# Performance work log

Hardware: AMD Instinct MI355X
Metric: run time of the kernel (lower is better)

## Reference

```python
import jax, jax.numpy as jnp
import numpy as np

TEMPERATURE = 0.5
SCALE_LOSS = 1.0 / 32.0
LAMBDA = 0.0039


def setup_inputs() -> dict:
    key = jax.random.key(0)
    z = jax.random.normal(key, (4096, 6, 256), dtype=jnp.float32)
    return {"z": z}


def reference(z):
    B, V = z.shape[0], z.shape[1]
    # [B, V, ...] -> [V, B, D], L2-normalize embeddings
    zv = z.reshape(B, V, -1).transpose(1, 0, 2)
    zn = zv / jnp.linalg.norm(zv, axis=-1, keepdims=True)

    # Positive error: per-sample cross-view similarity [B, V, V]
    sim_pos = jnp.einsum('vbd,wbd->bvw', zn, zn)
    pos = jnp.exp((1.0 - sim_pos) / TEMPERATURE).mean(axis=(1, 2))  # [B]

    # Negative error: per-view within-batch similarity [V, B, B]
    sim_neg = jnp.exp(jnp.einsum('vbd,vcd->vbc', zn, zn) / TEMPERATURE)
    offdiag_mask = ~jnp.eye(B, dtype=bool)  # [B, B]
    off_mean = jnp.where(offdiag_mask[None], sim_neg, 0.0).sum(-1) / (B - 1)  # [V, B]
    neg = off_mean.sum(0)  # [B], accumulated over views

    return jnp.sum(pos) * SCALE_LOSS + LAMBDA * jnp.sum(neg)
```

## Files before the change

### kernel.cpp

```cpp
#include <hip/hip_runtime.h>
#include <cstdint>
#include <cstddef>

#define B_N 4096
#define V_N 6
#define D_N 256
#define NTILE 528
#define NBLK (NTILE * V_N)

typedef int i32x4 __attribute__((ext_vector_type(4)));

#define QC 298.0f
#define INV_C2_X2 (2.0f / (QC * QC))

__device__ __forceinline__ void async_load16(void* lds, const void* gmem) {
  __builtin_amdgcn_global_load_lds(
      (const __attribute__((address_space(1))) unsigned int*)gmem,
      (__attribute__((address_space(3))) unsigned int*)lds,
      16, 0, 0);
}

__global__ __launch_bounds__(256) void norm_pos_kernel(
    const float* __restrict__ z, signed char* __restrict__ znb,
    float* __restrict__ pos_part) {
  const int lane = threadIdx.x & 63;
  const int w = threadIdx.x >> 6;
  const int b = blockIdx.x * 4 + w;

  const float4* zb4 = (const float4*)(z + (size_t)b * (V_N * D_N));
  float4 x[V_N];
#pragma unroll
  for (int v = 0; v < V_N; ++v) x[v] = zb4[v * 64 + lane];

  float s[21];
  {
    int p = 0;
#pragma unroll
    for (int v = 0; v < V_N; ++v)
#pragma unroll
      for (int u = v; u < V_N; ++u) {
        s[p] = x[v].x * x[u].x + x[v].y * x[u].y +
               x[v].z * x[u].z + x[v].w * x[u].w;
        ++p;
      }
  }
#pragma unroll
  for (int off = 1; off < 64; off <<= 1)
#pragma unroll
    for (int q = 0; q < 21; ++q)
      s[q] += __shfl_xor(s[q], off);

  const int selfidx[V_N] = {0, 6, 11, 15, 18, 20};
  float inv[V_N];
#pragma unroll
  for (int v = 0; v < V_N; ++v) inv[v] = rsqrtf(s[selfidx[v]]);

#pragma unroll
  for (int v = 0; v < V_N; ++v) {
    const float sc = inv[v] * QC;
    int q0 = (int)rintf(fminf(127.0f, fmaxf(-127.0f, x[v].x * sc)));
    int q1 = (int)rintf(fminf(127.0f, fmaxf(-127.0f, x[v].y * sc)));
    int q2 = (int)rintf(fminf(127.0f, fmaxf(-127.0f, x[v].z * sc)));
    int q3 = (int)rintf(fminf(127.0f, fmaxf(-127.0f, x[v].w * sc)));
    int packed = (q0 & 255) | ((q1 & 255) << 8) | ((q2 & 255) << 16)
               | ((q3 & 255) << 24);
    ((int*)(znb + ((size_t)v * B_N + b) * D_N))[lane] = packed;
  }

  float psum = 0.0f;
  {
    int p = 0;
#pragma unroll
    for (int v = 0; v < V_N; ++v)
#pragma unroll
      for (int u = v; u < V_N; ++u) {
        if (u > v) psum += __expf(2.0f * (1.0f - s[p] * inv[v] * inv[u]));
        ++p;
      }
  }
  if (lane == 0) pos_part[b] = psum;
}

__global__ __launch_bounds__(256) void gram_kernel(
    const signed char* __restrict__ znb, float* __restrict__ neg_part) {
  const int v = blockIdx.y;
  const int t = blockIdx.x;
  int i = (int)((sqrtf(8.0f * (float)t + 1.0f) - 1.0f) * 0.5f);
  while ((i + 1) * (i + 2) / 2 <= t) ++i;
  while (i * (i + 1) / 2 > t) --i;
  const int j = t - i * (i + 1) / 2;

  const signed char* Zv = znb + (size_t)v * B_N * D_N;
  const signed char* Ag = Zv + (size_t)(i * 128) * D_N;
  const signed char* Bg = Zv + (size_t)(j * 128) * D_N;

  __shared__ signed char As[128][128];
  __shared__ signed char Bs[128][128];
  __shared__ float blk[4];

  const int tid = threadIdx.x;
  const int lane = tid & 63;
  const int w = tid >> 6;
  const int wr = w >> 1;
  const int wc = w & 1;

  i32x4 c[4][4];
#pragma unroll
  for (int a = 0; a < 4; ++a)
#pragma unroll
    for (int b2 = 0; b2 < 4; ++b2) c[a][b2] = (i32x4){0, 0, 0, 0};

  const int kc = lane >> 4;
  const int mrow = wr * 64 + (lane & 15);
  const int ncol = wc * 64 + (lane & 15);

  signed char* AsF = &As[0][0];
  signed char* BsF = &Bs[0][0];

  for (int k0 = 0; k0 < D_N; k0 += 128) {
    __syncthreads();
#pragma unroll
    for (int q = 0; q < 4; ++q) {
      const int s = tid + 256 * q;
      const int row = s >> 3;
      const int gc = (s & 7) ^ (row & 7);
      async_load16(AsF + s * 16, Ag + (size_t)row * D_N + k0 + gc * 16);
      async_load16(BsF + s * 16, Bg + (size_t)row * D_N + k0 + gc * 16);
    }
    __syncthreads();

#pragma unroll
    for (int kk = 0; kk < 2; ++kk) {
      const int cbase = kk * 4 + kc;
      i32x4 af[4], bfr[4];
#pragma unroll
      for (int f = 0; f < 4; ++f) {
        const int ra = mrow + 16 * f;
        const int rb2 = ncol + 16 * f;
        af[f]  = *(const i32x4*)(AsF + ra * 128 + ((cbase ^ (ra & 7)) * 16));
        bfr[f] = *(const i32x4*)(BsF + rb2 * 128 + ((cbase ^ (rb2 & 7)) * 16));
      }
#pragma unroll
      for (int fm = 0; fm < 4; ++fm)
#pragma unroll
        for (int fn = 0; fn < 4; ++fn)
          c[fm][fn] = __builtin_amdgcn_mfma_i32_16x16x64_i8(
              af[fm], bfr[fn], c[fm][fn], 0, 0, 0);
    }
  }

  float lsum = 0.0f;
  const int rb = i * 128 + wr * 64 + (lane >> 4) * 4;
  const int cb = j * 128 + wc * 64 + (lane & 15);
#pragma unroll
  for (int fm = 0; fm < 4; ++fm) {
#pragma unroll
    for (int fn = 0; fn < 4; ++fn) {
      const int gcol = cb + fn * 16;
#pragma unroll
      for (int r = 0; r < 4; ++r) {
        const int grow = rb + fm * 16 + r;
        float e = __expf((float)c[fm][fn][r] * INV_C2_X2);
        lsum += (grow == gcol) ? 0.0f : e;
      }
    }
  }
  if (i != j) lsum *= 2.0f;

#pragma unroll
  for (int off = 32; off > 0; off >>= 1) lsum += __shfl_down(lsum, off);
  if (lane == 0) blk[w] = lsum;
  __syncthreads();
  if (tid == 0) neg_part[t + NTILE * v] = blk[0] + blk[1] + blk[2] + blk[3];
}

__global__ __launch_bounds__(1024) void finalize_kernel(
    const float* __restrict__ pos_part, const float* __restrict__ neg_part,
    float* __restrict__ out) {
  const int t = threadIdx.x;
  const int lane = t & 63;
  const int w = t >> 6;
  __shared__ float pr[16], nr[16];

  float p = 0.0f;
  for (int idx = t; idx < B_N; idx += 1024) p += pos_part[idx];
  float n = 0.0f;
  for (int idx = t; idx < NBLK; idx += 1024) n += neg_part[idx];
#pragma unroll
  for (int off = 32; off > 0; off >>= 1) {
    p += __shfl_down(p, off);
    n += __shfl_down(n, off);
  }
  if (lane == 0) { pr[w] = p; nr[w] = n; }
  __syncthreads();
  if (t == 0) {
    float P = 0.0f, N = 0.0f;
#pragma unroll
    for (int k = 0; k < 16; ++k) { P += pr[k]; N += nr[k]; }
    out[0] = (1.0f / 32.0f) * ((float)B_N / 6.0f + P / 18.0f) +
             0.0039f * (N / (float)(B_N - 1));
  }
}

extern "C" void kernel_launch(void* const* d_in, const int* in_sizes, int n_in,
                              void* d_out, int out_size, void* d_ws, size_t ws_size,
                              hipStream_t stream) {
  const float* z = (const float*)d_in[0];
  float* out = (float*)d_out;
  float* pos_part = (float*)d_ws;
  float* neg_part = (float*)((char*)d_ws + 16384);
  signed char* znb = (signed char*)((char*)d_ws + 32768);

  norm_pos_kernel<<<B_N / 4, 256, 0, stream>>>(z, znb, pos_part);
  dim3 grid(NTILE, V_N, 1);
  gram_kernel<<<grid, 256, 0, stream>>>(znb, neg_part);
  finalize_kernel<<<1, 1024, 0, stream>>>(pos_part, neg_part, out);
}
```

Baseline: 102.6 us.

## Process chunks of column tiles per block with resident A and double-buffered B

The gram kernel now launches 80 blocks per view instead of 528. Each block covers up to 8 column tiles of one row tile. The full 128x256 A tile stays resident in LDS, and B half-tiles are double-buffered with async loads overlapped with MFMA compute using manual waitcnt, barriers and priority hints. This cuts redundant A reloads and per-block launch and reduction overhead, and hides load latency. The cost is more LDS per block (64KB), fewer and unevenly loaded blocks (chunk sizes vary), and fragile hand-written vmcnt synchronization.

```diff
diff --git a/kernel.cpp b/kernel.cpp
--- a/kernel.cpp
+++ b/kernel.cpp
@@ -5,8 +5,9 @@
 #define B_N 4096
 #define V_N 6
 #define D_N 256
-#define NTILE 528
-#define NBLK (NTILE * V_N)
+#define CHUNK 8
+#define NCHUNK 80
+#define NNEG (NCHUNK * V_N)
 
 typedef int i32x4 __attribute__((ext_vector_type(4)));
 
@@ -81,21 +82,26 @@
   if (lane == 0) pos_part[b] = psum;
 }
 
-__global__ __launch_bounds__(256) void gram_kernel(
+__global__ __launch_bounds__(256, 2) void gram_kernel(
     const signed char* __restrict__ znb, float* __restrict__ neg_part) {
   const int v = blockIdx.y;
-  const int t = blockIdx.x;
-  int i = (int)((sqrtf(8.0f * (float)t + 1.0f) - 1.0f) * 0.5f);
-  while ((i + 1) * (i + 2) / 2 <= t) ++i;
-  while (i * (i + 1) / 2 > t) --i;
-  const int j = t - i * (i + 1) / 2;
+
+  int i = 31, rem = blockIdx.x;
+  for (int r = 31; r >= 0; --r) {
+    const int nc = (r + 8) >> 3;
+    if (rem < nc) { i = r; break; }
+    rem -= nc;
+  }
+  const int j0 = rem * CHUNK;
+  const int jend = min(j0 + CHUNK, i + 1);
+  const int T = jend - j0;
+  const int nsteps = 2 * T;
 
   const signed char* Zv = znb + (size_t)v * B_N * D_N;
   const signed char* Ag = Zv + (size_t)(i * 128) * D_N;
-  const signed char* Bg = Zv + (size_t)(j * 128) * D_N;
-
-  __shared__ signed char As[128][128];
-  __shared__ signed char Bs[128][128];
+
+  __shared__ signed char As[128][256];
+  __shared__ signed char Bs[2][128][128];
   __shared__ float blk[4];
 
   const int tid = threadIdx.x;
@@ -104,74 +110,120 @@
   const int wr = w >> 1;
   const int wc = w & 1;
 
-  i32x4 c[4][4];
-#pragma unroll
-  for (int a = 0; a < 4; ++a)
-#pragma unroll
-    for (int b2 = 0; b2 < 4; ++b2) c[a][b2] = (i32x4){0, 0, 0, 0};
-
   const int kc = lane >> 4;
   const int mrow = wr * 64 + (lane & 15);
   const int ncol = wc * 64 + (lane & 15);
 
   signed char* AsF = &As[0][0];
-  signed char* BsF = &Bs[0][0];
-
-  for (int k0 = 0; k0 < D_N; k0 += 128) {
-    __syncthreads();
-#pragma unroll
-    for (int q = 0; q < 4; ++q) {
-      const int s = tid + 256 * q;
-      const int row = s >> 3;
-      const int gc = (s & 7) ^ (row & 7);
-      async_load16(AsF + s * 16, Ag + (size_t)row * D_N + k0 + gc * 16);
-      async_load16(BsF + s * 16, Bg + (size_t)row * D_N + k0 + gc * 16);
+
+#pragma unroll
+  for (int q = 0; q < 8; ++q) {
+    const int sA = tid + 256 * q;
+    const int row = sA >> 4;
+    const int gc = (sA & 15) ^ (row & 15);
+    async_load16(AsF + sA * 16, Ag + (size_t)row * D_N + gc * 16);
+  }
+#pragma unroll
+  for (int st = 0; st < 2; ++st) {
+    if (st < nsteps) {
+      const int jn = j0 + (st >> 1), hn = st & 1;
+      const signed char* Bg = Zv + (size_t)(jn * 128) * D_N + hn * 128;
+      signed char* BsF = &Bs[st & 1][0][0];
+#pragma unroll
+      for (int q = 0; q < 4; ++q) {
+        const int s = tid + 256 * q;
+        const int row = s >> 3;
+        const int gc = (s & 7) ^ (row & 7);
+        async_load16(BsF + s * 16, Bg + (size_t)row * D_N + gc * 16);
+      }
     }
-    __syncthreads();
-
-#pragma unroll
-    for (int kk = 0; kk < 2; ++kk) {
-      const int cbase = kk * 4 + kc;
-      i32x4 af[4], bfr[4];
-#pragma unroll
-      for (int f = 0; f < 4; ++f) {
-        const int ra = mrow + 16 * f;
-        const int rb2 = ncol + 16 * f;
-        af[f]  = *(const i32x4*)(AsF + ra * 128 + ((cbase ^ (ra & 7)) * 16));
-        bfr[f] = *(const i32x4*)(BsF + rb2 * 128 + ((cbase ^ (rb2 & 7)) * 16));
-      }
-#pragma unroll
-      for (int fm = 0; fm < 4; ++fm)
-#pragma unroll
-        for (int fn = 0; fn < 4; ++fn)
-          c[fm][fn] = __builtin_amdgcn_mfma_i32_16x16x64_i8(
-              af[fm], bfr[fn], c[fm][fn], 0, 0, 0);
+  }
+  asm volatile("s_waitcnt vmcnt(4)" ::: "memory");
+  __builtin_amdgcn_sched_barrier(0);
+  __builtin_amdgcn_s_barrier();
+
+  float wsum = 0.0f;
+  int s = 0;
+  for (int jt = j0; jt < jend; ++jt) {
+    i32x4 c[4][4];
+#pragma unroll
+    for (int a = 0; a < 4; ++a)
+#pragma unroll
+      for (int b2 = 0; b2 < 4; ++b2) c[a][b2] = (i32x4){0, 0, 0, 0};
+
+#pragma unroll
+    for (int h = 0; h < 2; ++h, ++s) {
+      const signed char* BsF = &Bs[s & 1][0][0];
+      __builtin_amdgcn_s_setprio(1);
+#pragma unroll
+      for (int kk = 0; kk < 2; ++kk) {
+        const int cb8 = kk * 4 + kc;
+        const int ca16 = h * 8 + kk * 4 + kc;
+        i32x4 af[4], bfr[4];
+#pragma unroll
+        for (int f = 0; f < 4; ++f) {
+          const int ra = mrow + 16 * f;
+          const int rb = ncol + 16 * f;
+          af[f]  = *(const i32x4*)(AsF + ra * 256 + ((ca16 ^ (ra & 15)) * 16));
+          bfr[f] = *(const i32x4*)(BsF + rb * 128 + ((cb8 ^ (rb & 7)) * 16));
+        }
+#pragma unroll
+        for (int fm = 0; fm < 4; ++fm)
+#pragma unroll
+          for (int fn = 0; fn < 4; ++fn)
+            c[fm][fn] = __builtin_amdgcn_mfma_i32_16x16x64_i8(
+                af[fm], bfr[fn], c[fm][fn], 0, 0, 0);
+      }
+      __builtin_amdgcn_s_setprio(0);
+      __builtin_amdgcn_s_barrier();
+      const int sn = s + 2;
+      if (sn < nsteps) {
+        const int jn = j0 + (sn >> 1), hn = sn & 1;
+        const signed char* Bg = Zv + (size_t)(jn * 128) * D_N + hn * 128;
+        signed char* BsN = &Bs[s & 1][0][0];
+#pragma unroll
+        for (int q = 0; q < 4; ++q) {
+          const int sg = tid + 256 * q;
+          const int row = sg >> 3;
+          const int gc = (sg & 7) ^ (row & 7);
+          async_load16(BsN + sg * 16, Bg + (size_t)row * D_N + gc * 16);
+        }
+      }
+      if (h == 1) {
+        float tsum = 0.0f;
+        const int rb0 = i * 128 + wr * 64 + (lane >> 4) * 4;
+        const int cb0 = jt * 128 + wc * 64 + (lane & 15);
+#pragma unroll
+        for (int fm = 0; fm < 4; ++fm)
+#pragma unroll
+          for (int fn = 0; fn < 4; ++fn) {
+            const int gcol = cb0 + fn * 16;
+#pragma unroll
+            for (int r = 0; r < 4; ++r) {
+              const int grow = rb0 + fm * 16 + r;
+              float e = __expf((float)c[fm][fn][r] * INV_C2_X2);
+              tsum += (grow == gcol) ? 0.0f : e;
+            }
+          }
+        wsum += (i != jt) ? 2.0f * tsum : tsum;
+      }
+      if (sn < nsteps) {
+        asm volatile("s_waitcnt vmcnt(4)" ::: "memory");
+      } else {
+        asm volatile("s_waitcnt vmcnt(0)" ::: "memory");
+      }
+      __builtin_amdgcn_sched_barrier(0);
+      __builtin_amdgcn_s_barrier();
     }
   }
 
-  float lsum = 0.0f;
-  const int rb = i * 128 + wr * 64 + (lane >> 4) * 4;
-  const int cb = j * 128 + wc * 64 + (lane & 15);
-#pragma unroll
-  for (int fm = 0; fm < 4; ++fm) {
-#pragma unroll
-    for (int fn = 0; fn < 4; ++fn) {
-      const int gcol = cb + fn * 16;
-#pragma unroll
-      for (int r = 0; r < 4; ++r) {
-        const int grow = rb + fm * 16 + r;
-        float e = __expf((float)c[fm][fn][r] * INV_C2_X2);
-        lsum += (grow == gcol) ? 0.0f : e;
-      }
-    }
-  }
-  if (i != j) lsum *= 2.0f;
-
-#pragma unroll
-  for (int off = 32; off > 0; off >>= 1) lsum += __shfl_down(lsum, off);
-  if (lane == 0) blk[w] = lsum;
+#pragma unroll
+  for (int off = 32; off > 0; off >>= 1) wsum += __shfl_down(wsum, off);
+  if (lane == 0) blk[w] = wsum;
   __syncthreads();
-  if (tid == 0) neg_part[t + NTILE * v] = blk[0] + blk[1] + blk[2] + blk[3];
+  if (tid == 0)
+    neg_part[blockIdx.y * NCHUNK + blockIdx.x] =
+        blk[0] + blk[1] + blk[2] + blk[3];
 }
 
 __global__ __launch_bounds__(1024) void finalize_kernel(
@@ -185,7 +237,7 @@
   float p = 0.0f;
   for (int idx = t; idx < B_N; idx += 1024) p += pos_part[idx];
   float n = 0.0f;
-  for (int idx = t; idx < NBLK; idx += 1024) n += neg_part[idx];
+  for (int idx = t; idx < NNEG; idx += 1024) n += neg_part[idx];
 #pragma unroll
   for (int off = 32; off > 0; off >>= 1) {
     p += __shfl_down(p, off);
@@ -212,7 +264,7 @@
   signed char* znb = (signed char*)((char*)d_ws + 32768);
 
   norm_pos_kernel<<<B_N / 4, 256, 0, stream>>>(z, znb, pos_part);
-  dim3 grid(NTILE, V_N, 1);
+  dim3 grid(NCHUNK, V_N, 1);
   gram_kernel<<<grid, 256, 0, stream>>>(znb, neg_part);
   finalize_kernel<<<1, 1024, 0, stream>>>(pos_part, neg_part, out);
 }
```

New measurement: 102.4 us. About the same (-0.2%).
